# Kernel optimization log

Hardware: AMD Instinct MI355X
Metric: run time of the kernel (lower is better)

Reference implementation:

```python
import jax, jax.numpy as jnp
import numpy as np

DT = 1e-4   # self.dttt
DX = 1.0    # self.dxx
FRE = 100.0 # self.fre
PI = 3.1415926  # constant used literally in the torch code


def setup_inputs() -> dict:
    key = jax.random.key(0)
    k1, k2, k3, k4 = jax.random.split(key, 4)
    H = W = 512
    steps = 256  # coffe * bsize1
    output = jax.random.normal(k1, (steps + 2, 1, H, W), dtype=jnp.float32)
    c = jax.random.uniform(k2, (1, 1, H, W), dtype=jnp.float32)  # wave speed map
    loc_x = jax.random.randint(k3, (3,), 0, 510)
    loc_y = jax.random.randint(k4, (3,), 0, 510)
    return {"output": output, "c": c, "loc_x": loc_x, "loc_y": loc_y,
            "bsize1": 256, "id2": 1, "coffe": 1}


def reference(output, c, loc_x, loc_y, bsize1, id2, coffe):
    # FDTD rollout of get_phy_Loss2. output: [T,1,H,W]; c: [1,1,H,W].
    steps = int(coffe * bsize1)              # number of new frames produced
    cc = c[0, 0]                              # [H, W]
    r = (DT ** 2) * cc ** 2 / (DX ** 2)       # r1 == r2 since dx == dy
    src_mask = loc_x != -1                    # sources with loc_x == -1 are skipped

    def step(carry, n):
        prev, cur = carry                     # frames n-1 and n, each [H, W]
        lap = r[1:-1, 1:-1] * (
            (cur[2:, 1:-1] - 2.0 * cur[1:-1, 1:-1] + cur[:-2, 1:-1])
            + (cur[1:-1, 2:] - 2.0 * cur[1:-1, 1:-1] + cur[1:-1, :-2]))
        interior = 2.0 * cur[1:-1, 1:-1] - prev[1:-1, 1:-1] + lap
        new = jnp.zeros_like(cur).at[1:-1, 1:-1].set(interior)
        # source injection (after interior update, before boundary overwrite)
        src = 1500.0 * jnp.sin(2.0 * PI * FRE * (bsize1 * id2 + n + 1) * DT)
        new = new.at[loc_x, loc_y].set(
            jnp.where(src_mask, src, new[loc_x, loc_y]))
        # absorbing-style boundary updates, applied in the same order as torch:
        new = new.at[0, :].set(cur[0, :] - DT * cc[0, :] * (cur[0, :] - cur[1, :]) / DX)
        new = new.at[:, 0].set(cur[:, 0] - DT * cc[:, 0] * (cur[:, 0] - cur[:, 1]) / DX)
        new = new.at[:, -1].set(cur[:, -1] - DT * cc[:, -1] * (cur[:, -1] - cur[:, -2]) / DX)
        new = new.at[-1, :].set(cur[-1, :] - DT * cc[-1, :] * (cur[-1, :] - cur[-2, :]) / DX)
        return (cur, new), new

    ns = jnp.arange(1, steps + 1)
    _, ys = jax.lax.scan(step, (output[0, 0], output[1, 0]), ns)
    return ys[:, None, :, :]  # [steps, 1, H, W] == output3[2:] unsqueezed
```

## Files before the change

kernel.cpp:

```cpp
#include <hip/hip_runtime.h>


#define HH 512
#define WW 512
#define TILE 32
#define TS 16
#define NW 8
#define RPT 8
#define PHC ((float)(2.0 * 3.1415926 * 100.0))

#if __has_builtin(__builtin_amdgcn_update_dpp)
__device__ __forceinline__ float nbrL(float x) {
    int i = __builtin_bit_cast(int, x);
    i = __builtin_amdgcn_update_dpp(i, i, 0x138, 0xf, 0xf, false);
    return __builtin_bit_cast(float, i);
}
__device__ __forceinline__ float nbrR(float x) {
    int i = __builtin_bit_cast(int, x);
    i = __builtin_amdgcn_update_dpp(i, i, 0x130, 0xf, 0xf, false);
    return __builtin_bit_cast(float, i);
}
#else
__device__ __forceinline__ float nbrL(float x) { return __shfl_up(x, 1, 64); }
__device__ __forceinline__ float nbrR(float x) { return __shfl_down(x, 1, 64); }
#endif

__global__ __launch_bounds__(512)
void fdtd_dpp(const float* __restrict__ prevF,
              const float* __restrict__ curF,
              const float* __restrict__ cmap,
              const int* __restrict__ locx,
              const int* __restrict__ locy,
              const int* __restrict__ pb,
              const int* __restrict__ pid2,
              float* __restrict__ out,
              int t0, int nk)
{
    __shared__ float sb[2][NW][2][64];

    const int lane = threadIdx.x & 63;
    const int w    = threadIdx.x >> 6;
    const int bx   = blockIdx.x & 15;
    const int by   = blockIdx.x >> 4;
    const int gx0  = bx * TILE - TS;
    const int gy0  = by * TILE - TS;
    const int gc   = gx0 + lane;
    const int R    = w * RPT;

    const int lx0 = locx[0], ly0 = locy[0];
    const int lx1 = locx[1], ly1 = locy[1];
    const int lx2 = locx[2], ly2 = locy[2];
    const int Bn  = pb[0] * pid2[0];

    float cur[RPT], pv[RPT], rr[RPT], cv[RPT];
    bool  issrc[RPT];
    const bool colOK = (gc >= 0) & (gc < WW);

    #pragma unroll
    for (int j = 0; j < RPT; ++j) {
        const int gr = gy0 + R + j;
        float c = 0.f, ce = 0.f, pp = 0.f;
        if (colOK && gr >= 0 && gr < HH) {
            const int gi = gr * WW + gc;
            c  = cmap[gi];
            ce = curF[gi];
            pp = prevF[gi];
        }
        cur[j] = ce; pv[j] = pp; cv[j] = c;
        rr[j]  = 1.0e-8f * c * c;
        issrc[j] = (gr == lx0 && gc == ly0) || (gr == lx1 && gc == ly1) ||
                   (gr == lx2 && gc == ly2);
    }
    sb[0][w][0][lane] = cur[0];
    sb[0][w][1][lane] = cur[RPT - 1];
    __syncthreads();

    const int wup = (w == 0)      ? 0      : w - 1;
    const int sup = (w == 0)      ? 0      : 1;
    const int wdn = (w == NW - 1) ? NW - 1 : w + 1;
    const int sdn = (w == NW - 1) ? 1      : 0;

    const bool edge    = (bx == 0) | (bx == 15) | (by == 0) | (by == 15);
    const bool doStore = (w >= 2) & (w <= 5) & (lane >= 16) & (lane < 48);
    const size_t rowOff = (size_t)(gy0 + R) * WW + gc;

    if (!edge) {
        for (int k = 1; k <= nk; ++k) {
            const int p = (k - 1) & 1;
            const float srcv =
                1500.0f * __sinf(PHC * (float)(Bn + t0 + k + 1) * 1.0e-4f);
            const float upb = sb[p][wup][sup][lane];
            const float dnb = sb[p][wdn][sdn][lane];
            float nc[RPT];
            #pragma unroll
            for (int j = 0; j < RPT; ++j) {
                const float c = cur[j];
                const float u = (j == 0)       ? upb : cur[j - 1];
                const float d = (j == RPT - 1) ? dnb : cur[j + 1];
                const float l = nbrL(c);
                const float r = nbrR(c);
                float v = 2.f * c - pv[j] + rr[j] * (((u + d) + (l + r)) - 4.f * c);
                nc[j] = issrc[j] ? srcv : v;
            }
            sb[p ^ 1][w][0][lane] = nc[0];
            sb[p ^ 1][w][1][lane] = nc[RPT - 1];
            if (doStore) {
                float* op = out + (size_t)(t0 + k - 1) * (size_t)(HH * WW) + rowOff;
                #pragma unroll
                for (int j = 0; j < RPT; ++j) op[j * WW] = nc[j];
            }
            #pragma unroll
            for (int j = 0; j < RPT; ++j) { pv[j] = cur[j]; cur[j] = nc[j]; }
            __syncthreads();
        }
    } else {
        const bool isC0   = (gc == 0);
        const bool isC511 = (gc == WW - 1);
        for (int k = 1; k <= nk; ++k) {
            const int p = (k - 1) & 1;
            const float srcv =
                1500.0f * __sinf(PHC * (float)(Bn + t0 + k + 1) * 1.0e-4f);
            const float upb = sb[p][wup][sup][lane];
            const float dnb = sb[p][wdn][sdn][lane];
            float nc[RPT];
            #pragma unroll
            for (int j = 0; j < RPT; ++j) {
                const int gr = gy0 + R + j;
                const float c = cur[j];
                const float u = (j == 0)       ? upb : cur[j - 1];
                const float d = (j == RPT - 1) ? dnb : cur[j + 1];
                const float l = nbrL(c);
                const float r = nbrR(c);
                float v = 2.f * c - pv[j] + rr[j] * (((u + d) + (l + r)) - 4.f * c);
                v = issrc[j] ? srcv : v;
                if (gr == 0)      v = c - 1.0e-4f * cv[j] * (c - d);
                if (isC0)         v = c - 1.0e-4f * cv[j] * (c - r);
                if (isC511)       v = c - 1.0e-4f * cv[j] * (c - l);
                if (gr == HH - 1) v = c - 1.0e-4f * cv[j] * (c - u);
                nc[j] = v;
            }
            sb[p ^ 1][w][0][lane] = nc[0];
            sb[p ^ 1][w][1][lane] = nc[RPT - 1];
            if (doStore) {
                float* op = out + (size_t)(t0 + k - 1) * (size_t)(HH * WW) + rowOff;
                #pragma unroll
                for (int j = 0; j < RPT; ++j) op[j * WW] = nc[j];
            }
            #pragma unroll
            for (int j = 0; j < RPT; ++j) { pv[j] = cur[j]; cur[j] = nc[j]; }
            __syncthreads();
        }
    }
}

extern "C" void kernel_launch(void* const* d_in, const int* in_sizes, int n_in,
                              void* d_out, int out_size, void* d_ws, size_t ws_size,
                              hipStream_t stream) {
    const float* in_out = (const float*)d_in[0];
    const float* cmap   = (const float*)d_in[1];
    const int*   locx   = (const int*)d_in[2];
    const int*   locy   = (const int*)d_in[3];
    const int*   pb     = (const int*)d_in[4];
    const int*   pid2   = (const int*)d_in[5];
    float* out = (float*)d_out;

    const int HW = HH * WW;
    const int steps = out_size / HW;
    const int nblocks = (HH / TILE) * (WW / TILE);

    for (int t0 = 0; t0 < steps; t0 += TS) {
        const int nk = (steps - t0 < TS) ? (steps - t0) : TS;
        const float *prevF, *curF;
        if (t0 == 0) {
            prevF = in_out;
            curF  = in_out + HW;
        } else {
            prevF = out + (size_t)(t0 - 2) * HW;
            curF  = out + (size_t)(t0 - 1) * HW;
        }
        hipLaunchKernelGGL(fdtd_dpp, dim3(nblocks), dim3(512), 0, stream,
                           prevF, curF, cmap, locx, locy, pb, pid2, out, t0, nk);
    }
}
```

Baseline: 248.8 us.

## Use per-wave overlapping row windows to sync only every four timesteps

Each wave now holds a 16-row window: its 8 owned rows plus a 4-row halo above and below. It advances 4 timesteps locally, shrinking the valid region each step, then exchanges the halo rows (both current and previous frames) through shared memory with one barrier. This replaces the per-step block barrier and single-row halo exchange. The cost is redundant stencil work on halo rows, twice the register arrays, and a larger LDS exchange, which may reduce occupancy.

```diff
diff --git a/kernel.cpp b/kernel.cpp
--- a/kernel.cpp
+++ b/kernel.cpp
@@ -6,7 +6,8 @@
 #define TILE 32
 #define TS 16
 #define NW 8
-#define RPT 8
+#define WIN 16
+#define EE 4
 #define PHC ((float)(2.0 * 3.1415926 * 100.0))
 
 #if __has_builtin(__builtin_amdgcn_update_dpp)
@@ -25,8 +26,85 @@
 __device__ __forceinline__ float nbrR(float x) { return __shfl_down(x, 1, 64); }
 #endif
 
+typedef float (*XchPtr)[2][NW][2][EE][64];
+
+template<bool EDGE>
+__device__ __forceinline__ void run_steps(
+    float (&cur)[WIN], float (&pv)[WIN], const float (&rr)[WIN],
+    const float (&cv)[WIN], unsigned smask, unsigned m0, unsigned m511,
+    bool isC0, bool isC511, bool doStore, size_t rowOff,
+    float* __restrict__ out, int t0, int nk, int Bn, int w, int lane,
+    XchPtr xch)
+{
+    for (int kb = 0; kb < nk; kb += EE) {
+        #pragma unroll
+        for (int s = 1; s <= EE; ++s) {
+            const int k = kb + s;
+            if (k > nk) break;
+            const float srcv =
+                1500.0f * __sinf(PHC * (float)(Bn + t0 + k + 1) * 1.0e-4f);
+            float nc[WIN];
+            #pragma unroll
+            for (int i = 1; i < WIN - 1; ++i) {
+                if (i < s || i >= WIN - s) continue;
+                const float c = cur[i];
+                const float u = cur[i - 1];
+                const float d = cur[i + 1];
+                const float l = nbrL(c);
+                const float r = nbrR(c);
+                float v = 2.f * c - pv[i] +
+                          rr[i] * (((u + d) + (l + r)) - 4.f * c);
+                v = ((smask >> i) & 1u) ? srcv : v;
+                if (EDGE) {
+                    if ((m0 >> i) & 1u)   v = c - 1.0e-4f * cv[i] * (c - d);
+                    if (isC0)             v = c - 1.0e-4f * cv[i] * (c - r);
+                    if (isC511)           v = c - 1.0e-4f * cv[i] * (c - l);
+                    if ((m511 >> i) & 1u) v = c - 1.0e-4f * cv[i] * (c - u);
+                }
+                pv[i] = c;
+                nc[i] = v;
+            }
+            #pragma unroll
+            for (int i = 1; i < WIN - 1; ++i) {
+                if (i < s || i >= WIN - s) continue;
+                cur[i] = nc[i];
+            }
+            if (doStore) {
+                float* op = out + (size_t)(t0 + k - 1) * (size_t)(HH * WW) + rowOff;
+                #pragma unroll
+                for (int j = 0; j < 8; ++j) op[j * WW] = cur[EE + j];
+            }
+        }
+        if (kb + EE < nk) {
+            const int buf = (kb >> 2) & 1;
+            #pragma unroll
+            for (int j = 0; j < EE; ++j) {
+                xch[buf][0][w][0][j][lane] = cur[EE + j];
+                xch[buf][0][w][1][j][lane] = cur[EE + 4 + j];
+                xch[buf][1][w][0][j][lane] = pv[EE + j];
+                xch[buf][1][w][1][j][lane] = pv[EE + 4 + j];
+            }
+            __syncthreads();
+            if (w > 0) {
+                #pragma unroll
+                for (int j = 0; j < EE; ++j) {
+                    cur[j] = xch[buf][0][w - 1][1][j][lane];
+                    pv[j]  = xch[buf][1][w - 1][1][j][lane];
+                }
+            }
+            if (w < NW - 1) {
+                #pragma unroll
+                for (int j = 0; j < EE; ++j) {
+                    cur[12 + j] = xch[buf][0][w + 1][0][j][lane];
+                    pv[12 + j]  = xch[buf][1][w + 1][0][j][lane];
+                }
+            }
+        }
+    }
+}
+
 __global__ __launch_bounds__(512)
-void fdtd_dpp(const float* __restrict__ prevF,
+void fdtd_win(const float* __restrict__ prevF,
               const float* __restrict__ curF,
               const float* __restrict__ cmap,
               const int* __restrict__ locx,
@@ -36,7 +114,7 @@
               float* __restrict__ out,
               int t0, int nk)
 {
-    __shared__ float sb[2][NW][2][64];
+    __shared__ float xch[2][2][NW][2][EE][64];
 
     const int lane = threadIdx.x & 63;
     const int w    = threadIdx.x >> 6;
@@ -45,112 +123,44 @@
     const int gx0  = bx * TILE - TS;
     const int gy0  = by * TILE - TS;
     const int gc   = gx0 + lane;
-    const int R    = w * RPT;
+    const int B    = w * 8 - EE;
 
     const int lx0 = locx[0], ly0 = locy[0];
     const int lx1 = locx[1], ly1 = locy[1];
     const int lx2 = locx[2], ly2 = locy[2];
     const int Bn  = pb[0] * pid2[0];
 
-    float cur[RPT], pv[RPT], rr[RPT], cv[RPT];
-    bool  issrc[RPT];
+    float cur[WIN], pv[WIN], rr[WIN], cv[WIN];
+    unsigned smask = 0, m0 = 0, m511 = 0;
     const bool colOK = (gc >= 0) & (gc < WW);
 
     #pragma unroll
-    for (int j = 0; j < RPT; ++j) {
-        const int gr = gy0 + R + j;
+    for (int i = 0; i < WIN; ++i) {
+        const int gr = gy0 + B + i;
         float c = 0.f, ce = 0.f, pp = 0.f;
         if (colOK && gr >= 0 && gr < HH) {
             const int gi = gr * WW + gc;
-            c  = cmap[gi];
-            ce = curF[gi];
-            pp = prevF[gi];
+            c = cmap[gi]; ce = curF[gi]; pp = prevF[gi];
         }
-        cur[j] = ce; pv[j] = pp; cv[j] = c;
-        rr[j]  = 1.0e-8f * c * c;
-        issrc[j] = (gr == lx0 && gc == ly0) || (gr == lx1 && gc == ly1) ||
-                   (gr == lx2 && gc == ly2);
+        cur[i] = ce; pv[i] = pp; cv[i] = c; rr[i] = 1.0e-8f * c * c;
+        if ((gr == lx0 && gc == ly0) || (gr == lx1 && gc == ly1) ||
+            (gr == lx2 && gc == ly2)) smask |= (1u << i);
+        if (gr == 0)      m0   |= (1u << i);
+        if (gr == HH - 1) m511 |= (1u << i);
     }
-    sb[0][w][0][lane] = cur[0];
-    sb[0][w][1][lane] = cur[RPT - 1];
-    __syncthreads();
-
-    const int wup = (w == 0)      ? 0      : w - 1;
-    const int sup = (w == 0)      ? 0      : 1;
-    const int wdn = (w == NW - 1) ? NW - 1 : w + 1;
-    const int sdn = (w == NW - 1) ? 1      : 0;
 
     const bool edge    = (bx == 0) | (bx == 15) | (by == 0) | (by == 15);
+    const bool isC0    = (gc == 0);
+    const bool isC511  = (gc == WW - 1);
     const bool doStore = (w >= 2) & (w <= 5) & (lane >= 16) & (lane < 48);
-    const size_t rowOff = (size_t)(gy0 + R) * WW + gc;
+    const size_t rowOff = (size_t)(gy0 + w * 8) * WW + gc;
 
-    if (!edge) {
-        for (int k = 1; k <= nk; ++k) {
-            const int p = (k - 1) & 1;
-            const float srcv =
-                1500.0f * __sinf(PHC * (float)(Bn + t0 + k + 1) * 1.0e-4f);
-            const float upb = sb[p][wup][sup][lane];
-            const float dnb = sb[p][wdn][sdn][lane];
-            float nc[RPT];
-            #pragma unroll
-            for (int j = 0; j < RPT; ++j) {
-                const float c = cur[j];
-                const float u = (j == 0)       ? upb : cur[j - 1];
-                const float d = (j == RPT - 1) ? dnb : cur[j + 1];
-                const float l = nbrL(c);
-                const float r = nbrR(c);
-                float v = 2.f * c - pv[j] + rr[j] * (((u + d) + (l + r)) - 4.f * c);
-                nc[j] = issrc[j] ? srcv : v;
-            }
-            sb[p ^ 1][w][0][lane] = nc[0];
-            sb[p ^ 1][w][1][lane] = nc[RPT - 1];
-            if (doStore) {
-                float* op = out + (size_t)(t0 + k - 1) * (size_t)(HH * WW) + rowOff;
-                #pragma unroll
-                for (int j = 0; j < RPT; ++j) op[j * WW] = nc[j];
-            }
-            #pragma unroll
-            for (int j = 0; j < RPT; ++j) { pv[j] = cur[j]; cur[j] = nc[j]; }
-            __syncthreads();
-        }
-    } else {
-        const bool isC0   = (gc == 0);
-        const bool isC511 = (gc == WW - 1);
-        for (int k = 1; k <= nk; ++k) {
-            const int p = (k - 1) & 1;
-            const float srcv =
-                1500.0f * __sinf(PHC * (float)(Bn + t0 + k + 1) * 1.0e-4f);
-            const float upb = sb[p][wup][sup][lane];
-            const float dnb = sb[p][wdn][sdn][lane];
-            float nc[RPT];
-            #pragma unroll
-            for (int j = 0; j < RPT; ++j) {
-                const int gr = gy0 + R + j;
-                const float c = cur[j];
-                const float u = (j == 0)       ? upb : cur[j - 1];
-                const float d = (j == RPT - 1) ? dnb : cur[j + 1];
-                const float l = nbrL(c);
-                const float r = nbrR(c);
-                float v = 2.f * c - pv[j] + rr[j] * (((u + d) + (l + r)) - 4.f * c);
-                v = issrc[j] ? srcv : v;
-                if (gr == 0)      v = c - 1.0e-4f * cv[j] * (c - d);
-                if (isC0)         v = c - 1.0e-4f * cv[j] * (c - r);
-                if (isC511)       v = c - 1.0e-4f * cv[j] * (c - l);
-                if (gr == HH - 1) v = c - 1.0e-4f * cv[j] * (c - u);
-                nc[j] = v;
-            }
-            sb[p ^ 1][w][0][lane] = nc[0];
-            sb[p ^ 1][w][1][lane] = nc[RPT - 1];
-            if (doStore) {
-                float* op = out + (size_t)(t0 + k - 1) * (size_t)(HH * WW) + rowOff;
-                #pragma unroll
-                for (int j = 0; j < RPT; ++j) op[j * WW] = nc[j];
-            }
-            #pragma unroll
-            for (int j = 0; j < RPT; ++j) { pv[j] = cur[j]; cur[j] = nc[j]; }
-            __syncthreads();
-        }
-    }
+    if (!edge)
+        run_steps<false>(cur, pv, rr, cv, smask, m0, m511, isC0, isC511,
+                         doStore, rowOff, out, t0, nk, Bn, w, lane, xch);
+    else
+        run_steps<true>(cur, pv, rr, cv, smask, m0, m511, isC0, isC511,
+                        doStore, rowOff, out, t0, nk, Bn, w, lane, xch);
 }
 
 extern "C" void kernel_launch(void* const* d_in, const int* in_sizes, int n_in,
@@ -178,7 +188,7 @@
             prevF = out + (size_t)(t0 - 2) * HW;
             curF  = out + (size_t)(t0 - 1) * HW;
         }
-        hipLaunchKernelGGL(fdtd_dpp, dim3(nblocks), dim3(512), 0, stream,
+        hipLaunchKernelGGL(fdtd_win, dim3(nblocks), dim3(512), 0, stream,
                            prevF, curF, cmap, locx, locy, pb, pid2, out, t0, nk);
     }
 }
```

New measurement: 321.4 us. 1.29x slower.

## Shrink row tiles to raise block count and skip inactive halo waves

Applied to the files above, without the earlier changes.

Changes tiles from 32x32 to 8 rows by 32 columns with 5 waves per block, quadrupling the number of blocks so more waves are resident across CUs. Interior blocks skip computing waves whose halo rows have already become invalid at the current time step. Boundary row checks are precomputed into bitmasks. The trade-off is much larger redundant halo computation per output row and more global reloads of the halo.

```diff
diff --git a/kernel.cpp b/kernel.cpp
--- a/kernel.cpp
+++ b/kernel.cpp
@@ -3,9 +3,10 @@
 
 #define HH 512
 #define WW 512
-#define TILE 32
+#define TR 8
+#define TC 32
 #define TS 16
-#define NW 8
+#define NW 5
 #define RPT 8
 #define PHC ((float)(2.0 * 3.1415926 * 100.0))
 
@@ -25,8 +26,8 @@
 __device__ __forceinline__ float nbrR(float x) { return __shfl_down(x, 1, 64); }
 #endif
 
-__global__ __launch_bounds__(512)
-void fdtd_dpp(const float* __restrict__ prevF,
+__global__ __launch_bounds__(320, 5)
+void fdtd_occ(const float* __restrict__ prevF,
               const float* __restrict__ curF,
               const float* __restrict__ cmap,
               const int* __restrict__ locx,
@@ -42,8 +43,8 @@
     const int w    = threadIdx.x >> 6;
     const int bx   = blockIdx.x & 15;
     const int by   = blockIdx.x >> 4;
-    const int gx0  = bx * TILE - TS;
-    const int gy0  = by * TILE - TS;
+    const int gx0  = bx * TC - TS;
+    const int gy0  = by * TR - TS;
     const int gc   = gx0 + lane;
     const int R    = w * RPT;
 
@@ -54,6 +55,7 @@
 
     float cur[RPT], pv[RPT], rr[RPT], cv[RPT];
     bool  issrc[RPT];
+    unsigned m0 = 0, m511 = 0;
     const bool colOK = (gc >= 0) & (gc < WW);
 
     #pragma unroll
@@ -70,6 +72,8 @@
         rr[j]  = 1.0e-8f * c * c;
         issrc[j] = (gr == lx0 && gc == ly0) || (gr == lx1 && gc == ly1) ||
                    (gr == lx2 && gc == ly2);
+        if (gr == 0)      m0   |= (1u << j);
+        if (gr == HH - 1) m511 |= (1u << j);
     }
     sb[0][w][0][lane] = cur[0];
     sb[0][w][1][lane] = cur[RPT - 1];
@@ -80,11 +84,47 @@
     const int wdn = (w == NW - 1) ? NW - 1 : w + 1;
     const int sdn = (w == NW - 1) ? 1      : 0;
 
-    const bool edge    = (bx == 0) | (bx == 15) | (by == 0) | (by == 15);
-    const bool doStore = (w >= 2) & (w <= 5) & (lane >= 16) & (lane < 48);
-    const size_t rowOff = (size_t)(gy0 + R) * WW + gc;
+    const bool edge    = (bx == 0) | (bx == 15) | (by <= 2) | (by >= 61);
+    const bool doStore = (w == 2) & (lane >= 16) & (lane < 48);
+    const size_t rowOff = (size_t)(gy0 + 2 * RPT) * WW + gc;
 
     if (!edge) {
+        for (int k = 1; k <= nk; ++k) {
+            const int p = (k - 1) & 1;
+            const bool active = (R + RPT > k) & (R < NW * RPT - k);
+            if (active) {
+                const float srcv =
+                    1500.0f * __sinf(PHC * (float)(Bn + t0 + k + 1) * 1.0e-4f);
+                const float upb = sb[p][wup][sup][lane];
+                const float dnb = sb[p][wdn][sdn][lane];
+                float nc[RPT];
+                #pragma unroll
+                for (int j = 0; j < RPT; ++j) {
+                    const float c = cur[j];
+                    const float u = (j == 0)       ? upb : cur[j - 1];
+                    const float d = (j == RPT - 1) ? dnb : cur[j + 1];
+                    const float l = nbrL(c);
+                    const float r = nbrR(c);
+                    float v = 2.f * c - pv[j] +
+                              rr[j] * (((u + d) + (l + r)) - 4.f * c);
+                    nc[j] = issrc[j] ? srcv : v;
+                }
+                sb[p ^ 1][w][0][lane] = nc[0];
+                sb[p ^ 1][w][1][lane] = nc[RPT - 1];
+                if (doStore) {
+                    float* op = out + (size_t)(t0 + k - 1) * (size_t)(HH * WW)
+                                    + rowOff;
+                    #pragma unroll
+                    for (int j = 0; j < RPT; ++j) op[j * WW] = nc[j];
+                }
+                #pragma unroll
+                for (int j = 0; j < RPT; ++j) { pv[j] = cur[j]; cur[j] = nc[j]; }
+            }
+            __syncthreads();
+        }
+    } else {
+        const bool isC0   = (gc == 0);
+        const bool isC511 = (gc == WW - 1);
         for (int k = 1; k <= nk; ++k) {
             const int p = (k - 1) & 1;
             const float srcv =
@@ -99,50 +139,20 @@
                 const float d = (j == RPT - 1) ? dnb : cur[j + 1];
                 const float l = nbrL(c);
                 const float r = nbrR(c);
-                float v = 2.f * c - pv[j] + rr[j] * (((u + d) + (l + r)) - 4.f * c);
-                nc[j] = issrc[j] ? srcv : v;
-            }
-            sb[p ^ 1][w][0][lane] = nc[0];
-            sb[p ^ 1][w][1][lane] = nc[RPT - 1];
-            if (doStore) {
-                float* op = out + (size_t)(t0 + k - 1) * (size_t)(HH * WW) + rowOff;
-                #pragma unroll
-                for (int j = 0; j < RPT; ++j) op[j * WW] = nc[j];
-            }
-            #pragma unroll
-            for (int j = 0; j < RPT; ++j) { pv[j] = cur[j]; cur[j] = nc[j]; }
-            __syncthreads();
-        }
-    } else {
-        const bool isC0   = (gc == 0);
-        const bool isC511 = (gc == WW - 1);
-        for (int k = 1; k <= nk; ++k) {
-            const int p = (k - 1) & 1;
-            const float srcv =
-                1500.0f * __sinf(PHC * (float)(Bn + t0 + k + 1) * 1.0e-4f);
-            const float upb = sb[p][wup][sup][lane];
-            const float dnb = sb[p][wdn][sdn][lane];
-            float nc[RPT];
-            #pragma unroll
-            for (int j = 0; j < RPT; ++j) {
-                const int gr = gy0 + R + j;
-                const float c = cur[j];
-                const float u = (j == 0)       ? upb : cur[j - 1];
-                const float d = (j == RPT - 1) ? dnb : cur[j + 1];
-                const float l = nbrL(c);
-                const float r = nbrR(c);
-                float v = 2.f * c - pv[j] + rr[j] * (((u + d) + (l + r)) - 4.f * c);
+                float v = 2.f * c - pv[j] +
+                          rr[j] * (((u + d) + (l + r)) - 4.f * c);
                 v = issrc[j] ? srcv : v;
-                if (gr == 0)      v = c - 1.0e-4f * cv[j] * (c - d);
-                if (isC0)         v = c - 1.0e-4f * cv[j] * (c - r);
-                if (isC511)       v = c - 1.0e-4f * cv[j] * (c - l);
-                if (gr == HH - 1) v = c - 1.0e-4f * cv[j] * (c - u);
+                if ((m0 >> j) & 1u)   v = c - 1.0e-4f * cv[j] * (c - d);
+                if (isC0)             v = c - 1.0e-4f * cv[j] * (c - r);
+                if (isC511)           v = c - 1.0e-4f * cv[j] * (c - l);
+                if ((m511 >> j) & 1u) v = c - 1.0e-4f * cv[j] * (c - u);
                 nc[j] = v;
             }
             sb[p ^ 1][w][0][lane] = nc[0];
             sb[p ^ 1][w][1][lane] = nc[RPT - 1];
             if (doStore) {
-                float* op = out + (size_t)(t0 + k - 1) * (size_t)(HH * WW) + rowOff;
+                float* op = out + (size_t)(t0 + k - 1) * (size_t)(HH * WW)
+                                + rowOff;
                 #pragma unroll
                 for (int j = 0; j < RPT; ++j) op[j * WW] = nc[j];
             }
@@ -166,7 +176,7 @@
 
     const int HW = HH * WW;
     const int steps = out_size / HW;
-    const int nblocks = (HH / TILE) * (WW / TILE);
+    const int nblocks = (WW / TC) * (HH / TR);
 
     for (int t0 = 0; t0 < steps; t0 += TS) {
         const int nk = (steps - t0 < TS) ? (steps - t0) : TS;
@@ -178,7 +188,7 @@
             prevF = out + (size_t)(t0 - 2) * HW;
             curF  = out + (size_t)(t0 - 1) * HW;
         }
-        hipLaunchKernelGGL(fdtd_dpp, dim3(nblocks), dim3(512), 0, stream,
+        hipLaunchKernelGGL(fdtd_occ, dim3(nblocks), dim3(320), 0, stream,
                            prevF, curF, cmap, locx, locy, pb, pid2, out, t0, nk);
     }
 }
```

Result: slower. 521.2 us (+109.4%).
